# Kernel optimization log

Measured on AMD Instinct MI355X. Metric: run time of the kernel, lower is better.

## Reference

```python
import jax, jax.numpy as jnp
import numpy as np

MASK_FILL = jnp.float32(-2**32 + 1)

def dice(x, alpha):
    # x: (S, B, F); batch-dim (dim=0) mean/std, unbiased std like torch.std
    avg = x.mean(axis=0)
    std = jnp.std(x, axis=0, ddof=1)
    p = jax.nn.sigmoid((x - avg) / std)
    return x * p + alpha * x * (1.0 - p)

def setup_inputs() -> dict:
    key = jax.random.key(0)
    ks = jax.random.split(key, 12)
    S, B, D = 200, 1024, 128          # seq_len, batch, 2H
    F = 4 * D                          # num_features = 512
    L1, L2 = 80, 40
    inp = {
        "query": jax.random.normal(ks[0], (B, D), jnp.float32),
        "facts": jax.random.normal(ks[1], (S, B, D), jnp.float32),
        "mask": jax.random.randint(ks[2], (S, B), 0, 2).astype(bool),
        "W1": jax.random.normal(ks[3], (F, L1), jnp.float32) / np.sqrt(F),
        "b1": jnp.zeros((L1,), jnp.float32),
        "a1": jnp.zeros((1,), jnp.float32),
        "W2": jax.random.normal(ks[4], (L1, L2), jnp.float32) / np.sqrt(L1),
        "b2": jnp.zeros((L2,), jnp.float32),
        "a2": jnp.zeros((1,), jnp.float32),
        "W3": jax.random.normal(ks[5], (L2, 1), jnp.float32) / np.sqrt(L2),
        "b3": jnp.zeros((1,), jnp.float32),
    }
    return inp

def reference(query, facts, mask, W1, b1, a1, W2, b2, a2, W3, b3):
    S, B, D = facts.shape
    # faithful to torch: tile along feature dim then reshape (permutes elements)
    q2 = jnp.tile(query, (1, S)).reshape(S, B, D)
    x = jnp.concatenate([q2, facts, q2 * facts, q2 - facts], axis=-1)  # (S,B,4D)
    h = dice(jnp.einsum('sbf,fl->sbl', x, W1) + b1, a1)
    h = dice(jnp.einsum('sbf,fl->sbl', h, W2) + b2, a2)
    logits = (jnp.einsum('sbf,fl->sbl', h, W3) + b3).squeeze(-1)  # (S,B)
    masked = jnp.where(mask, logits, MASK_FILL)
    normalized = jax.nn.softmax(masked, axis=0)
    return normalized[..., None] * facts  # (S,B,D)
```

## Files before the change

### kernel.cpp

```cpp
#include <hip/hip_runtime.h>
#include <hip/hip_bf16.h>
#include <math.h>

#define SS 200
#define BB 1024
#define DD 128
#define FF 512
#define LL1 80
#define LL2 40
#define PP (SS*BB)
#define MASK_FILL_F (-4294967295.0f)

typedef short bf16x8 __attribute__((ext_vector_type(8)));
typedef float f32x4  __attribute__((ext_vector_type(4)));

static __device__ __forceinline__ unsigned short f2bf(float x) {
    __hip_bfloat16 h = __float2bfloat16(x);
    return *reinterpret_cast<unsigned short*>(&h);
}
static __device__ __forceinline__ float bf2f(unsigned short u) {
    __hip_bfloat16 h = *reinterpret_cast<__hip_bfloat16*>(&u);
    return __bfloat162float(h);
}
static __device__ __forceinline__ void split8(const float* x, bf16x8& ah, bf16x8& al) {
#pragma unroll
    for (int j = 0; j < 8; ++j) {
        unsigned u = __float_as_uint(x[j]);
        ah[j] = (short)(u >> 16);
        float hi = __uint_as_float(u & 0xffff0000u);
        al[j] = (short)f2bf(x[j] - hi);
    }
}

__global__ void k_prep_all(const float* __restrict__ W1, const float* __restrict__ W2,
                           const unsigned char* __restrict__ mask,
                           unsigned short* __restrict__ bfr1,
                           unsigned short* __restrict__ bfr2, int* __restrict__ flag) {
    const int blk = blockIdx.x;
    if (blk == 35) {
        if (threadIdx.x == 0) {
            int f = 0;
            for (int i = 0; i < 256; ++i)
                if ((i & 3) && mask[i]) f = 1;
            *flag = f;
        }
        return;
    }
    if (blk < 30) {
        int t = blk * 256 + threadIdx.x;
        if (t >= 120 * 64) return;
        int lane = t & 63;
        int fid  = t >> 6;
        int nt   = fid % 5;
        int kt   = (fid / 5) & 3;
        int hl   = (fid / 20) & 1;
        int seg  = fid / 40;
        int n     = nt * 16 + (lane & 15);
        int kbase = kt * 32 + (lane >> 4) * 8;
        unsigned short* o = bfr1 + (size_t)t * 8;
#pragma unroll
        for (int j = 0; j < 8; ++j) {
            int k = kbase + j;
            float w;
            if (seg == 0)      w = W1[k * LL1 + n] + W1[(384 + k) * LL1 + n];
            else if (seg == 1) w = W1[(128 + k) * LL1 + n] - W1[(384 + k) * LL1 + n];
            else               w = W1[(256 + k) * LL1 + n];
            unsigned short hb = f2bf(w);
            o[j] = (hl == 0) ? hb : f2bf(w - bf2f(hb));
        }
    } else {
        int t = (blk - 30) * 256 + threadIdx.x;
        if (t >= 18 * 64) return;
        int lane = t & 63;
        int fid  = t >> 6;
        int hl   = fid & 1;
        int nt   = (fid >> 1) % 3;
        int kt   = fid / 6;
        int n  = nt * 16 + (lane & 15);
        int kb = kt * 32 + (lane >> 4) * 8;
        unsigned short* o = bfr2 + (size_t)t * 8;
#pragma unroll
        for (int j = 0; j < 8; ++j) {
            int k = kb + j;
            float w = (k < LL1 && n < LL2) ? W2[k * LL2 + n] : 0.f;
            unsigned short hb = f2bf(w);
            o[j] = (hl == 0) ? hb : f2bf(w - bf2f(hb));
        }
    }
}

__global__ __launch_bounds__(256, 3) void k1_mfma(
    const float* __restrict__ query, const float* __restrict__ facts,
    const unsigned short* __restrict__ bfr, const float* __restrict__ b1,
    float* __restrict__ z1) {
    const int tid  = threadIdx.x;
    const int lane = tid & 63;
    const int m    = lane & 15;
    const int quad = lane >> 4;
    const int pw   = blockIdx.x * 128 + (tid >> 6) * 32;

    f32x4 acc[2][5];
#pragma unroll
    for (int t = 0; t < 2; ++t)
#pragma unroll
        for (int nt = 0; nt < 5; ++nt) acc[t][nt] = (f32x4){0.f, 0.f, 0.f, 0.f};

    int pr[2], qr[2];
#pragma unroll
    for (int t = 0; t < 2; ++t) {
        pr[t] = pw + t * 16 + m;
        qr[t] = pr[t] / SS;
    }

#pragma unroll
    for (int kt = 0; kt < 4; ++kt) {
        const int dbase = kt * 32 + quad * 8;
        float q8[2][8], f8[2][8];
#pragma unroll
        for (int t = 0; t < 2; ++t) {
            *(float4*)&q8[t][0] = *(const float4*)(query + (size_t)qr[t] * DD + dbase);
            *(float4*)&q8[t][4] = *(const float4*)(query + (size_t)qr[t] * DD + dbase + 4);
            *(float4*)&f8[t][0] = *(const float4*)(facts + (size_t)pr[t] * DD + dbase);
            *(float4*)&f8[t][4] = *(const float4*)(facts + (size_t)pr[t] * DD + dbase + 4);
        }
#pragma unroll
        for (int seg = 0; seg < 3; ++seg) {
            bf16x8 Bh[5], Bl[5];
            const unsigned short* bh0 = bfr + ((((size_t)(seg * 2 + 0) * 4 + kt) * 5) * 64 + lane) * 8;
            const unsigned short* bl0 = bfr + ((((size_t)(seg * 2 + 1) * 4 + kt) * 5) * 64 + lane) * 8;
#pragma unroll
            for (int nt = 0; nt < 5; ++nt) {
                Bh[nt] = *(const bf16x8*)(bh0 + (size_t)nt * 512);
                Bl[nt] = *(const bf16x8*)(bl0 + (size_t)nt * 512);
            }
            bf16x8 ah[2], al[2];
#pragma unroll
            for (int t = 0; t < 2; ++t) {
                float x8[8];
#pragma unroll
                for (int j = 0; j < 8; ++j)
                    x8[j] = (seg == 0) ? q8[t][j] : (seg == 1 ? f8[t][j] : q8[t][j] * f8[t][j]);
                split8(x8, ah[t], al[t]);
            }
#pragma unroll
            for (int t = 0; t < 2; ++t)
#pragma unroll
                for (int nt = 0; nt < 5; ++nt) {
                    acc[t][nt] = __builtin_amdgcn_mfma_f32_16x16x32_bf16(ah[t], Bh[nt], acc[t][nt], 0, 0, 0);
                    acc[t][nt] = __builtin_amdgcn_mfma_f32_16x16x32_bf16(al[t], Bh[nt], acc[t][nt], 0, 0, 0);
                    acc[t][nt] = __builtin_amdgcn_mfma_f32_16x16x32_bf16(ah[t], Bl[nt], acc[t][nt], 0, 0, 0);
                }
        }
    }
#pragma unroll
    for (int t = 0; t < 2; ++t)
#pragma unroll
        for (int nt = 0; nt < 5; ++nt) {
            int n = nt * 16 + m;
            float bias = b1[n];
#pragma unroll
            for (int r = 0; r < 4; ++r)
                z1[(size_t)(pw + t * 16 + quad * 4 + r) * LL1 + n] = acc[t][nt][r] + bias;
        }
}

__global__ __launch_bounds__(256) void k_stats(
    const float* __restrict__ z, int C,
    float* __restrict__ sum, float* __restrict__ sumsq) {
    int col = blockIdx.x * 256 + threadIdx.x;
    int s0  = blockIdx.y * 25;
    const float* pz = z + (size_t)s0 * C + col;
    float ps = 0.f, pss = 0.f;
#pragma unroll 5
    for (int i = 0; i < 25; ++i) {
        float v = pz[(size_t)i * C];
        ps += v;
        pss = fmaf(v, v, pss);
    }
    atomicAdd(&sum[col], ps);
    atomicAdd(&sumsq[col], pss);
}

__global__ __launch_bounds__(256, 3) void k2_mfma(
    const float* __restrict__ z1, const float* __restrict__ sum1,
    const float* __restrict__ sumsq1, const float* __restrict__ a1,
    const unsigned short* __restrict__ bfr2, const float* __restrict__ b2,
    float* __restrict__ z2T) {
    const int tid  = threadIdx.x;
    const int lane = tid & 63;
    const int m    = lane & 15;
    const int quad = lane >> 4;
    const int pw   = blockIdx.x * 128 + (tid >> 6) * 32;
    const float alpha = *a1;

    bf16x8 Bh[3][3], Bl[3][3];
#pragma unroll
    for (int kt = 0; kt < 3; ++kt)
#pragma unroll
        for (int nt = 0; nt < 3; ++nt) {
            Bh[kt][nt] = *(const bf16x8*)(bfr2 + (((size_t)(kt * 3 + nt) * 2 + 0) * 64 + lane) * 8);
            Bl[kt][nt] = *(const bf16x8*)(bfr2 + (((size_t)(kt * 3 + nt) * 2 + 1) * 64 + lane) * 8);
        }
    float b2v[3];
#pragma unroll
    for (int nt = 0; nt < 3; ++nt) {
        int n = nt * 16 + m;
        b2v[nt] = (n < LL2) ? b2[n] : 0.f;
    }

#pragma unroll
    for (int t = 0; t < 2; ++t) {
        const int p = pw + t * 16 + m;
        const int b = p & (BB - 1);
        f32x4 acc[3];
#pragma unroll
        for (int nt = 0; nt < 3; ++nt) acc[nt] = (f32x4){0.f, 0.f, 0.f, 0.f};

#pragma unroll
        for (int kt = 0; kt < 3; ++kt) {
            float x8[8];
            const int kb = kt * 32 + quad * 8;
            if (kt < 2 || quad < 2) {
                const float* zr = z1     + (size_t)p * LL1 + kb;
                const float* su = sum1   + (size_t)b * LL1 + kb;
                const float* sq = sumsq1 + (size_t)b * LL1 + kb;
                float vv[8], sv[8], qv[8];
                *(float4*)&vv[0] = *(const float4*)zr;
                *(float4*)&vv[4] = *(const float4*)(zr + 4);
                *(float4*)&sv[0] = *(const float4*)su;
                *(float4*)&sv[4] = *(const float4*)(su + 4);
                *(float4*)&qv[0] = *(const float4*)sq;
                *(float4*)&qv[4] = *(const float4*)(sq + 4);
#pragma unroll
                for (int j = 0; j < 8; ++j) {
                    float mean = sv[j] * (1.f / SS);
                    float var  = (qv[j] - (float)SS * mean * mean) * (1.f / (SS - 1));
                    float istd = rsqrtf(var);
                    float pp   = 1.f / (1.f + expf(-(vv[j] - mean) * istd));
                    x8[j] = vv[j] * (pp + alpha * (1.f - pp));
                }
            } else {
#pragma unroll
                for (int j = 0; j < 8; ++j) x8[j] = 0.f;
            }
            bf16x8 ah, al;
            split8(x8, ah, al);
#pragma unroll
            for (int nt = 0; nt < 3; ++nt) {
                acc[nt] = __builtin_amdgcn_mfma_f32_16x16x32_bf16(ah, Bh[kt][nt], acc[nt], 0, 0, 0);
                acc[nt] = __builtin_amdgcn_mfma_f32_16x16x32_bf16(al, Bh[kt][nt], acc[nt], 0, 0, 0);
                acc[nt] = __builtin_amdgcn_mfma_f32_16x16x32_bf16(ah, Bl[kt][nt], acc[nt], 0, 0, 0);
            }
        }
#pragma unroll
        for (int r = 0; r < 4; ++r) {
            const int prow = pw + t * 16 + quad * 4 + r;
            const int br = prow & (BB - 1);
            const int sr = prow >> 10;
            float* o = z2T + (size_t)br * (SS * LL2) + (size_t)sr * LL2;
#pragma unroll
            for (int nt = 0; nt < 3; ++nt) {
                int n = nt * 16 + m;
                if (n < LL2) o[n] = acc[nt][r] + b2v[nt];
            }
        }
    }
}

__global__ __launch_bounds__(256) void k3_fused(
    const float* __restrict__ z2T, const float* __restrict__ a2,
    const float* __restrict__ W3, const float* __restrict__ b3,
    const void* __restrict__ mask, const int* __restrict__ flag,
    float* __restrict__ wbufT) {
    const int b   = blockIdx.x;
    const int tid = threadIdx.x;
    __shared__ float lds[SS * 41];
    __shared__ float psum[6 * LL2], pssq[6 * LL2];
    __shared__ float smean[LL2], sistd[LL2], sw3[LL2];
    __shared__ float red[4];

    const float4* src = (const float4*)(z2T + (size_t)b * (SS * LL2));
    for (int i = tid; i < (SS * LL2) / 4; i += 256) {
        float4 v = src[i];
        int s = i / 10;
        int o = (i - s * 10) * 4;
        float* d = &lds[s * 41 + o];
        d[0] = v.x; d[1] = v.y; d[2] = v.z; d[3] = v.w;
    }
    __syncthreads();
    if (tid < 240) {
        int l = tid % LL2, c = tid / LL2;
        int s0 = c * 34, s1 = (c == 5) ? SS : s0 + 34;
        float sum = 0.f, ssq = 0.f;
        for (int s = s0; s < s1; ++s) {
            float v = lds[s * 41 + l];
            sum += v;
            ssq = fmaf(v, v, ssq);
        }
        psum[c * LL2 + l] = sum;
        pssq[c * LL2 + l] = ssq;
    }
    __syncthreads();
    if (tid < LL2) {
        float sum = 0.f, ssq = 0.f;
#pragma unroll
        for (int c = 0; c < 6; ++c) {
            sum += psum[c * LL2 + tid];
            ssq += pssq[c * LL2 + tid];
        }
        float mean = sum * (1.f / SS);
        float var  = (ssq - (float)SS * mean * mean) * (1.f / (SS - 1));
        smean[tid] = mean;
        sistd[tid] = rsqrtf(var);
        sw3[tid]   = W3[tid];
    }
    __syncthreads();
    const float alpha = *a2;
    const int boolLayout = *flag;

    float logit = -3.0e38f;
    if (tid < SS) {
        float dot = b3[0];
#pragma unroll
        for (int k = 0; k < LL2; ++k) {
            float v  = lds[tid * 41 + k];
            float pp = 1.f / (1.f + expf(-(v - smean[k]) * sistd[k]));
            float h  = v * (pp + alpha * (1.f - pp));
            dot = fmaf(h, sw3[k], dot);
        }
        int mi = tid * BB + b;
        bool mk = boolLayout ? (((const unsigned char*)mask)[mi] != 0)
                             : (((const int*)mask)[mi] != 0);
        logit = mk ? dot : MASK_FILL_F;
    }
    float v = logit;
#pragma unroll
    for (int off = 1; off < 64; off <<= 1) v = fmaxf(v, __shfl_xor(v, off, 64));
    if ((tid & 63) == 0) red[tid >> 6] = v;
    __syncthreads();
    float smax = fmaxf(fmaxf(red[0], red[1]), fmaxf(red[2], red[3]));
    __syncthreads();
    float e = (tid < SS) ? expf(logit - smax) : 0.f;
    v = e;
#pragma unroll
    for (int off = 1; off < 64; off <<= 1) v += __shfl_xor(v, off, 64);
    if ((tid & 63) == 0) red[tid >> 6] = v;
    __syncthreads();
    float inv = 1.f / (red[0] + red[1] + red[2] + red[3]);
    if (tid < SS) wbufT[(size_t)b * SS + tid] = e * inv;
}

__global__ __launch_bounds__(256) void k4_scale(
    const float* __restrict__ wbufT, const float* __restrict__ facts,
    float* __restrict__ out) {
    int i = blockIdx.x * 256 + threadIdx.x;
    int p = i >> 5;
    float w = wbufT[(size_t)(p & (BB - 1)) * SS + (p >> 10)];
    float4 f = ((const float4*)facts)[i];
    float4 o;
    o.x = f.x * w; o.y = f.y * w; o.z = f.z * w; o.w = f.w * w;
    ((float4*)out)[i] = o;
}

extern "C" void kernel_launch(void* const* d_in, const int* in_sizes, int n_in,
                              void* d_out, int out_size, void* d_ws, size_t ws_size,
                              hipStream_t stream) {
    const float* query = (const float*)d_in[0];
    const float* facts = (const float*)d_in[1];
    const void*  mask  = d_in[2];
    const float* W1 = (const float*)d_in[3];
    const float* b1 = (const float*)d_in[4];
    const float* a1 = (const float*)d_in[5];
    const float* W2 = (const float*)d_in[6];
    const float* b2 = (const float*)d_in[7];
    const float* a2 = (const float*)d_in[8];
    const float* W3 = (const float*)d_in[9];
    const float* b3 = (const float*)d_in[10];
    float* out = (float*)d_out;

    float* z1  = out;
    float* z2T = out + (size_t)PP * LL1;
    float* sum1   = out + 24576000;
    float* sumsq1 = out + 24657920;
    unsigned short* bfr1 = (unsigned short*)(out + 24739840);
    unsigned short* bfr2 = (unsigned short*)(out + 24801280);
    float* wbufT = (float*)d_ws;
    int*   flag  = (int*)((char*)d_ws + 900 * 1024);

    k_prep_all<<<36, 256, 0, stream>>>(W1, W2, (const unsigned char*)mask, bfr1, bfr2, flag);
    hipMemsetAsync(sum1, 0, 163840 * sizeof(float), stream);
    k1_mfma<<<PP / 128, 256, 0, stream>>>(query, facts, bfr1, b1, z1);
    k_stats<<<dim3((BB * LL1) / 256, 8), 256, 0, stream>>>(z1, BB * LL1, sum1, sumsq1);
    k2_mfma<<<PP / 128, 256, 0, stream>>>(z1, sum1, sumsq1, a1, bfr2, b2, z2T);
    k3_fused<<<BB, 256, 0, stream>>>(z2T, a2, W3, b3, mask, flag, wbufT);
    k4_scale<<<(PP * DD) / (256 * 4), 256, 0, stream>>>(wbufT, facts, out);
}
```

Before: 355.6 us.

## Stage MFMA weight fragments in LDS and precompute layer-1 mean/istd

k1 now copies the reordered bf16 hi/lo W1 fragments into shared memory in two halves, and each wave reads them from LDS instead of global/L2. The prep kernel's fragment order changes to match. k2 likewise stages W2 fragments in LDS and interleaves the two row tiles per k-step. The atomic-based stats kernel and its memset are replaced by a single-pass column kernel that writes mean and inverse std directly, so k2 no longer recomputes them per element. Occupancy hints change (k1 to 2 blocks per CU, k2 to 4). The stats kernel now has fewer blocks, each with a longer serial loop, and k1 adds barriers and a 60KB LDS footprint.

```diff
diff --git a/kernel.cpp b/kernel.cpp
--- a/kernel.cpp
+++ b/kernel.cpp
@@ -52,9 +52,12 @@
         int lane = t & 63;
         int fid  = t >> 6;
         int nt   = fid % 5;
-        int kt   = (fid / 5) & 3;
-        int hl   = (fid / 20) & 1;
-        int seg  = fid / 40;
+        int hl   = (fid / 5) % 2;
+        int step = (fid / 10) % 6;
+        int h    = fid / 60;
+        int ktL  = step / 3;
+        int seg  = step - 3 * ktL;
+        int kt   = h * 2 + ktL;
         int n     = nt * 16 + (lane & 15);
         int kbase = kt * 32 + (lane >> 4) * 8;
         unsigned short* o = bfr1 + (size_t)t * 8;
@@ -89,7 +92,7 @@
     }
 }
 
-__global__ __launch_bounds__(256, 3) void k1_mfma(
+__global__ __launch_bounds__(256, 2) void k1_mfma(
     const float* __restrict__ query, const float* __restrict__ facts,
     const unsigned short* __restrict__ bfr, const float* __restrict__ b1,
     float* __restrict__ z1) {
@@ -99,6 +102,8 @@
     const int quad = lane >> 4;
     const int pw   = blockIdx.x * 128 + (tid >> 6) * 32;
 
+    __shared__ unsigned short lbuf[30720];
+
     f32x4 acc[2][5];
 #pragma unroll
     for (int t = 0; t < 2; ++t)
@@ -112,44 +117,61 @@
         qr[t] = pr[t] / SS;
     }
 
-#pragma unroll
-    for (int kt = 0; kt < 4; ++kt) {
-        const int dbase = kt * 32 + quad * 8;
-        float q8[2][8], f8[2][8];
-#pragma unroll
-        for (int t = 0; t < 2; ++t) {
-            *(float4*)&q8[t][0] = *(const float4*)(query + (size_t)qr[t] * DD + dbase);
-            *(float4*)&q8[t][4] = *(const float4*)(query + (size_t)qr[t] * DD + dbase + 4);
-            *(float4*)&f8[t][0] = *(const float4*)(facts + (size_t)pr[t] * DD + dbase);
-            *(float4*)&f8[t][4] = *(const float4*)(facts + (size_t)pr[t] * DD + dbase + 4);
-        }
-#pragma unroll
-        for (int seg = 0; seg < 3; ++seg) {
-            bf16x8 Bh[5], Bl[5];
-            const unsigned short* bh0 = bfr + ((((size_t)(seg * 2 + 0) * 4 + kt) * 5) * 64 + lane) * 8;
-            const unsigned short* bl0 = bfr + ((((size_t)(seg * 2 + 1) * 4 + kt) * 5) * 64 + lane) * 8;
-#pragma unroll
-            for (int nt = 0; nt < 5; ++nt) {
-                Bh[nt] = *(const bf16x8*)(bh0 + (size_t)nt * 512);
-                Bl[nt] = *(const bf16x8*)(bl0 + (size_t)nt * 512);
-            }
-            bf16x8 ah[2], al[2];
+    float q8[2][2][8], f8[2][2][8];
+
+#pragma unroll 1
+    for (int h = 0; h < 2; ++h) {
+#pragma unroll
+        for (int ktL = 0; ktL < 2; ++ktL) {
+            const int dbase = (h * 2 + ktL) * 32 + quad * 8;
 #pragma unroll
             for (int t = 0; t < 2; ++t) {
-                float x8[8];
-#pragma unroll
-                for (int j = 0; j < 8; ++j)
-                    x8[j] = (seg == 0) ? q8[t][j] : (seg == 1 ? f8[t][j] : q8[t][j] * f8[t][j]);
-                split8(x8, ah[t], al[t]);
-            }
-#pragma unroll
-            for (int t = 0; t < 2; ++t)
+                *(float4*)&q8[ktL][t][0] = *(const float4*)(query + (size_t)qr[t] * DD + dbase);
+                *(float4*)&q8[ktL][t][4] = *(const float4*)(query + (size_t)qr[t] * DD + dbase + 4);
+                *(float4*)&f8[ktL][t][0] = *(const float4*)(facts + (size_t)pr[t] * DD + dbase);
+                *(float4*)&f8[ktL][t][4] = *(const float4*)(facts + (size_t)pr[t] * DD + dbase + 4);
+            }
+        }
+        if (h) __syncthreads();
+        {
+            const int4* src = (const int4*)bfr + h * 3840 + tid;
+#pragma unroll
+            for (int it = 0; it < 15; ++it) {
+                int4 v = src[it * 256];
+                *(int4*)((char*)lbuf + it * 4096 + tid * 16) = v;
+            }
+        }
+        __syncthreads();
+
+#pragma unroll
+        for (int ktL = 0; ktL < 2; ++ktL) {
+#pragma unroll
+            for (int seg = 0; seg < 3; ++seg) {
+                const int step = ktL * 3 + seg;
+                bf16x8 Bh[5], Bl[5];
 #pragma unroll
                 for (int nt = 0; nt < 5; ++nt) {
-                    acc[t][nt] = __builtin_amdgcn_mfma_f32_16x16x32_bf16(ah[t], Bh[nt], acc[t][nt], 0, 0, 0);
-                    acc[t][nt] = __builtin_amdgcn_mfma_f32_16x16x32_bf16(al[t], Bh[nt], acc[t][nt], 0, 0, 0);
-                    acc[t][nt] = __builtin_amdgcn_mfma_f32_16x16x32_bf16(ah[t], Bl[nt], acc[t][nt], 0, 0, 0);
+                    Bh[nt] = *(const bf16x8*)&lbuf[((step * 2 + 0) * 5 + nt) * 512 + lane * 8];
+                    Bl[nt] = *(const bf16x8*)&lbuf[((step * 2 + 1) * 5 + nt) * 512 + lane * 8];
                 }
+#pragma unroll
+                for (int t = 0; t < 2; ++t) {
+                    float x8[8];
+#pragma unroll
+                    for (int j = 0; j < 8; ++j)
+                        x8[j] = (seg == 0) ? q8[ktL][t][j]
+                              : (seg == 1 ? f8[ktL][t][j]
+                                          : q8[ktL][t][j] * f8[ktL][t][j]);
+                    bf16x8 ah, al;
+                    split8(x8, ah, al);
+#pragma unroll
+                    for (int nt = 0; nt < 5; ++nt) {
+                        acc[t][nt] = __builtin_amdgcn_mfma_f32_16x16x32_bf16(ah, Bh[nt], acc[t][nt], 0, 0, 0);
+                        acc[t][nt] = __builtin_amdgcn_mfma_f32_16x16x32_bf16(al, Bh[nt], acc[t][nt], 0, 0, 0);
+                        acc[t][nt] = __builtin_amdgcn_mfma_f32_16x16x32_bf16(ah, Bl[nt], acc[t][nt], 0, 0, 0);
+                    }
+                }
+            }
         }
     }
 #pragma unroll
@@ -164,26 +186,26 @@
         }
 }
 
-__global__ __launch_bounds__(256) void k_stats(
-    const float* __restrict__ z, int C,
-    float* __restrict__ sum, float* __restrict__ sumsq) {
-    int col = blockIdx.x * 256 + threadIdx.x;
-    int s0  = blockIdx.y * 25;
-    const float* pz = z + (size_t)s0 * C + col;
-    float ps = 0.f, pss = 0.f;
-#pragma unroll 5
-    for (int i = 0; i < 25; ++i) {
-        float v = pz[(size_t)i * C];
-        ps += v;
-        pss = fmaf(v, v, pss);
-    }
-    atomicAdd(&sum[col], ps);
-    atomicAdd(&sumsq[col], pss);
-}
-
-__global__ __launch_bounds__(256, 3) void k2_mfma(
-    const float* __restrict__ z1, const float* __restrict__ sum1,
-    const float* __restrict__ sumsq1, const float* __restrict__ a1,
+__global__ __launch_bounds__(256) void k_msd(
+    const float* __restrict__ z, float* __restrict__ mean, float* __restrict__ istd) {
+    const int col = blockIdx.x * 256 + threadIdx.x;
+    const float* p = z + col;
+    float s = 0.f, q = 0.f;
+#pragma unroll 10
+    for (int i = 0; i < SS; ++i) {
+        float v = p[(size_t)i * (BB * LL1)];
+        s += v;
+        q = fmaf(v, v, q);
+    }
+    float mn = s * (1.f / SS);
+    float var = (q - (float)SS * mn * mn) * (1.f / (SS - 1));
+    mean[col] = mn;
+    istd[col] = rsqrtf(var);
+}
+
+__global__ __launch_bounds__(256, 4) void k2_mfma(
+    const float* __restrict__ z1, const float* __restrict__ mean1,
+    const float* __restrict__ istd1, const float* __restrict__ a1,
     const unsigned short* __restrict__ bfr2, const float* __restrict__ b2,
     float* __restrict__ z2T) {
     const int tid  = threadIdx.x;
@@ -193,14 +215,17 @@
     const int pw   = blockIdx.x * 128 + (tid >> 6) * 32;
     const float alpha = *a1;
 
-    bf16x8 Bh[3][3], Bl[3][3];
-#pragma unroll
-    for (int kt = 0; kt < 3; ++kt)
-#pragma unroll
-        for (int nt = 0; nt < 3; ++nt) {
-            Bh[kt][nt] = *(const bf16x8*)(bfr2 + (((size_t)(kt * 3 + nt) * 2 + 0) * 64 + lane) * 8);
-            Bl[kt][nt] = *(const bf16x8*)(bfr2 + (((size_t)(kt * 3 + nt) * 2 + 1) * 64 + lane) * 8);
-        }
+    __shared__ unsigned short lb2[9216];
+    for (int i = tid; i < 1152; i += 256)
+        ((int4*)lb2)[i] = ((const int4*)bfr2)[i];
+    __syncthreads();
+
+    f32x4 acc[2][3];
+#pragma unroll
+    for (int t = 0; t < 2; ++t)
+#pragma unroll
+        for (int nt = 0; nt < 3; ++nt) acc[t][nt] = (f32x4){0.f, 0.f, 0.f, 0.f};
+
     float b2v[3];
 #pragma unroll
     for (int nt = 0; nt < 3; ++nt) {
@@ -209,35 +234,35 @@
     }
 
 #pragma unroll
-    for (int t = 0; t < 2; ++t) {
-        const int p = pw + t * 16 + m;
-        const int b = p & (BB - 1);
-        f32x4 acc[3];
-#pragma unroll
-        for (int nt = 0; nt < 3; ++nt) acc[nt] = (f32x4){0.f, 0.f, 0.f, 0.f};
-
-#pragma unroll
-        for (int kt = 0; kt < 3; ++kt) {
+    for (int kt = 0; kt < 3; ++kt) {
+        bf16x8 Bh[3], Bl[3];
+#pragma unroll
+        for (int nt = 0; nt < 3; ++nt) {
+            Bh[nt] = *(const bf16x8*)&lb2[((kt * 3 + nt) * 2 + 0) * 512 + lane * 8];
+            Bl[nt] = *(const bf16x8*)&lb2[((kt * 3 + nt) * 2 + 1) * 512 + lane * 8];
+        }
+        const int kb = kt * 32 + quad * 8;
+        const bool live = (kt < 2 || quad < 2);
+#pragma unroll
+        for (int t = 0; t < 2; ++t) {
+            const int p = pw + t * 16 + m;
+            const int b = p & (BB - 1);
             float x8[8];
-            const int kb = kt * 32 + quad * 8;
-            if (kt < 2 || quad < 2) {
-                const float* zr = z1     + (size_t)p * LL1 + kb;
-                const float* su = sum1   + (size_t)b * LL1 + kb;
-                const float* sq = sumsq1 + (size_t)b * LL1 + kb;
-                float vv[8], sv[8], qv[8];
+            if (live) {
+                const float* zr = z1    + (size_t)p * LL1 + kb;
+                const float* mu = mean1 + (size_t)b * LL1 + kb;
+                const float* is = istd1 + (size_t)b * LL1 + kb;
+                float vv[8], mv[8], iv[8];
                 *(float4*)&vv[0] = *(const float4*)zr;
                 *(float4*)&vv[4] = *(const float4*)(zr + 4);
-                *(float4*)&sv[0] = *(const float4*)su;
-                *(float4*)&sv[4] = *(const float4*)(su + 4);
-                *(float4*)&qv[0] = *(const float4*)sq;
-                *(float4*)&qv[4] = *(const float4*)(sq + 4);
+                *(float4*)&mv[0] = *(const float4*)mu;
+                *(float4*)&mv[4] = *(const float4*)(mu + 4);
+                *(float4*)&iv[0] = *(const float4*)is;
+                *(float4*)&iv[4] = *(const float4*)(is + 4);
 #pragma unroll
                 for (int j = 0; j < 8; ++j) {
-                    float mean = sv[j] * (1.f / SS);
-                    float var  = (qv[j] - (float)SS * mean * mean) * (1.f / (SS - 1));
-                    float istd = rsqrtf(var);
-                    float pp   = 1.f / (1.f + expf(-(vv[j] - mean) * istd));
-                    x8[j] = vv[j] * (pp + alpha * (1.f - pp));
+                    float pp = 1.f / (1.f + expf(-(vv[j] - mv[j]) * iv[j]));
+                    x8[j] = vv[j] * (alpha + (1.f - alpha) * pp);
                 }
             } else {
 #pragma unroll
@@ -247,11 +272,14 @@
             split8(x8, ah, al);
 #pragma unroll
             for (int nt = 0; nt < 3; ++nt) {
-                acc[nt] = __builtin_amdgcn_mfma_f32_16x16x32_bf16(ah, Bh[kt][nt], acc[nt], 0, 0, 0);
-                acc[nt] = __builtin_amdgcn_mfma_f32_16x16x32_bf16(al, Bh[kt][nt], acc[nt], 0, 0, 0);
-                acc[nt] = __builtin_amdgcn_mfma_f32_16x16x32_bf16(ah, Bl[kt][nt], acc[nt], 0, 0, 0);
-            }
-        }
+                acc[t][nt] = __builtin_amdgcn_mfma_f32_16x16x32_bf16(ah, Bh[nt], acc[t][nt], 0, 0, 0);
+                acc[t][nt] = __builtin_amdgcn_mfma_f32_16x16x32_bf16(al, Bh[nt], acc[t][nt], 0, 0, 0);
+                acc[t][nt] = __builtin_amdgcn_mfma_f32_16x16x32_bf16(ah, Bl[nt], acc[t][nt], 0, 0, 0);
+            }
+        }
+    }
+#pragma unroll
+    for (int t = 0; t < 2; ++t)
 #pragma unroll
         for (int r = 0; r < 4; ++r) {
             const int prow = pw + t * 16 + quad * 4 + r;
@@ -261,10 +289,9 @@
 #pragma unroll
             for (int nt = 0; nt < 3; ++nt) {
                 int n = nt * 16 + m;
-                if (n < LL2) o[n] = acc[nt][r] + b2v[nt];
-            }
-        }
-    }
+                if (n < LL2) o[n] = acc[t][nt][r] + b2v[nt];
+            }
+        }
 }
 
 __global__ __launch_bounds__(256) void k3_fused(
@@ -380,18 +407,17 @@
 
     float* z1  = out;
     float* z2T = out + (size_t)PP * LL1;
-    float* sum1   = out + 24576000;
-    float* sumsq1 = out + 24657920;
+    float* mean1 = out + 24576000;
+    float* istd1 = out + 24657920;
     unsigned short* bfr1 = (unsigned short*)(out + 24739840);
     unsigned short* bfr2 = (unsigned short*)(out + 24801280);
     float* wbufT = (float*)d_ws;
     int*   flag  = (int*)((char*)d_ws + 900 * 1024);
 
     k_prep_all<<<36, 256, 0, stream>>>(W1, W2, (const unsigned char*)mask, bfr1, bfr2, flag);
-    hipMemsetAsync(sum1, 0, 163840 * sizeof(float), stream);
     k1_mfma<<<PP / 128, 256, 0, stream>>>(query, facts, bfr1, b1, z1);
-    k_stats<<<dim3((BB * LL1) / 256, 8), 256, 0, stream>>>(z1, BB * LL1, sum1, sumsq1);
-    k2_mfma<<<PP / 128, 256, 0, stream>>>(z1, sum1, sumsq1, a1, bfr2, b2, z2T);
+    k_msd<<<(BB * LL1) / 256, 256, 0, stream>>>(z1, mean1, istd1);
+    k2_mfma<<<PP / 128, 256, 0, stream>>>(z1, mean1, istd1, a1, bfr2, b2, z2T);
     k3_fused<<<BB, 256, 0, stream>>>(z2T, a2, W3, b3, mask, flag, wbufT);
     k4_scale<<<(PP * DD) / (256 * 4), 256, 0, stream>>>(wbufT, facts, out);
 }
```

After: 311.7 us. 12.3% less time.
